# Kernel optimization log

Measured on AMD Instinct MI355X. Metric: run time of the kernel, lower is better.

The kernel has to match this reference:

```python
import jax, jax.numpy as jnp
import numpy as np

T, B, V, H = 2048, 32, 512, 512


def setup_inputs() -> dict:
    key = jax.random.key(0)
    ks = jax.random.split(key, 7)
    s = 1.0 / np.sqrt(V + H)  # torch nn.Linear default init bound
    u = lambda k, shape: jax.random.uniform(k, shape, jnp.float32, -s, s)
    return {
        "inputs": jax.random.normal(ks[0], (T, B, V), jnp.float32),
        "state": jnp.zeros((1, B, H), jnp.float32),
        "W_reset": u(ks[1], (V + H, H)),
        "b_reset": u(ks[2], (H,)),
        "W_net": u(ks[3], (V + H, H)),
        "b_net": u(ks[4], (H,)),
        "W_update": u(ks[5], (V + H, H)),
        "b_update": u(ks[6], (H,)),
    }


def reference(inputs, state, W_reset, b_reset, W_net, b_net, W_update, b_update):
    # inputs: [T, B, V], state: [1, B, H]
    h0 = state[0]  # [B, H]

    def step(h, x):
        # x: [B, V], h: [B, H]
        xh = jnp.concatenate([x, h], axis=-1)               # [B, V+H]
        R = jax.nn.sigmoid(xh @ W_reset + b_reset)          # [B, H]
        xr = jnp.concatenate([x, h * R], axis=-1)           # [B, V+H]
        H_t = jnp.tanh(xr @ W_net + b_net)                  # candidate
        Z = jax.nn.sigmoid(xr @ W_update + b_update)        # NOTE: from (x, h*R), faithful to source
        h_new = Z * h + (1.0 - Z) * H_t
        return h_new, h_new

    h_final, states = jax.lax.scan(step, h0, inputs)        # states: [T, B, H]
    return states, h_final[None]                            # ([T,B,H], [1,B,H])
```

## Files before the change

kernel.cpp:

```cpp
#include <hip/hip_runtime.h>
#include <cstdint>
#include <cstddef>

#define T_STEPS 2048
#define BATCH   32
#define VDIM    512
#define HDIM    512
#define SLICES  8
#define COLS    64
#define KPT     64
#define BM      128
#define BN      64

typedef _Float16 half2v __attribute__((ext_vector_type(2)));
typedef _Float16 half8v __attribute__((ext_vector_type(8)));
typedef float    f32x4  __attribute__((ext_vector_type(4)));

__device__ __forceinline__ float dot2h(half2v a, half2v b, float c) {
#if __has_builtin(__builtin_amdgcn_fdot2)
    return __builtin_amdgcn_fdot2(a, b, c, false);
#else
    return fmaf((float)a.x, (float)b.x, fmaf((float)a.y, (float)b.y, c));
#endif
}

__device__ __forceinline__ unsigned long long loadt(const unsigned long long* p) {
    return __hip_atomic_load(p, __ATOMIC_RELAXED, __HIP_MEMORY_SCOPE_AGENT);
}
__device__ __forceinline__ void storet(unsigned long long* p, float v, unsigned tag) {
    unsigned long long x = ((unsigned long long)tag << 32) | (unsigned)__float_as_uint(v);
    __hip_atomic_store(p, x, __ATOMIC_RELAXED, __HIP_MEMORY_SCOPE_AGENT);
}

__global__ __launch_bounds__(256)
void xproj_mfma(const float* __restrict__ X,
                const float* __restrict__ W0, const float* __restrict__ b0,
                const float* __restrict__ W1, const float* __restrict__ b1,
                const float* __restrict__ W2, const float* __restrict__ b2,
                float* __restrict__ xp, int M)
{
    const int g  = blockIdx.x >> 3;
    const int n0 = (blockIdx.x & 7) * BN;
    const int m0 = blockIdx.y * BM;
    const float* W    = (g == 0) ? W0 : (g == 1) ? W1 : W2;
    const float* bias = (g == 0) ? b0 : (g == 1) ? b1 : b2;
    float* out = xp + (size_t)g * M * HDIM;

    __shared__ __align__(16) _Float16 Blds[64 * 64 * 8];

    const int tid  = threadIdx.x;
    const int lane = tid & 63;
    const int w    = tid >> 6;
    const int r16  = lane & 15;
    const int kq   = lane >> 4;

    {
        const int c = tid & 63;
        #pragma unroll
        for (int it = 0; it < 16; ++it) {
            const int kg = (tid >> 6) + 4 * it;
            const float* src = W + (size_t)(kg * 8) * HDIM + n0 + c;
            half8v v;
            #pragma unroll
            for (int i = 0; i < 8; ++i) v[i] = (_Float16)src[(size_t)i * HDIM];
            *(half8v*)&Blds[(size_t)(kg * 64 + c) * 8] = v;
        }
    }
    __syncthreads();

    f32x4 acc[2][4] = {};

    for (int ks = 0; ks < 16; ++ks) {
        const int kg = 4 * ks + kq;
        half8v a[2];
        #pragma unroll
        for (int ms = 0; ms < 2; ++ms) {
            const float* ap = X + (size_t)(m0 + 32 * w + 16 * ms + r16) * VDIM + kg * 8;
            float4 a0 = *(const float4*)ap;
            float4 a1 = *(const float4*)(ap + 4);
            a[ms][0] = (_Float16)a0.x; a[ms][1] = (_Float16)a0.y;
            a[ms][2] = (_Float16)a0.z; a[ms][3] = (_Float16)a0.w;
            a[ms][4] = (_Float16)a1.x; a[ms][5] = (_Float16)a1.y;
            a[ms][6] = (_Float16)a1.z; a[ms][7] = (_Float16)a1.w;
        }
        #pragma unroll
        for (int cb = 0; cb < 4; ++cb) {
            half8v bf = *(const half8v*)&Blds[(size_t)(kg * 64 + 16 * cb + r16) * 8];
            acc[0][cb] = __builtin_amdgcn_mfma_f32_16x16x32_f16(a[0], bf, acc[0][cb], 0, 0, 0);
            acc[1][cb] = __builtin_amdgcn_mfma_f32_16x16x32_f16(a[1], bf, acc[1][cb], 0, 0, 0);
        }
    }

    #pragma unroll
    for (int cb = 0; cb < 4; ++cb) {
        const float bb = bias[n0 + 16 * cb + r16];
        #pragma unroll
        for (int ms = 0; ms < 2; ++ms)
            #pragma unroll
            for (int r = 0; r < 4; ++r) {
                const int row = m0 + 32 * w + 16 * ms + 4 * kq + r;
                out[(size_t)row * HDIM + n0 + 16 * cb + r16] = acc[ms][cb][r] + bb;
            }
    }
}

__global__ __launch_bounds__(512)
__attribute__((amdgpu_waves_per_eu(2, 2)))
void gru_scan3(const float* __restrict__ xp,
               const float* __restrict__ Wrh, const float* __restrict__ Wnh,
               const float* __restrict__ Wzh,
               const float* __restrict__ state, float* __restrict__ out,
               unsigned long long* __restrict__ hT,
               unsigned long long* __restrict__ uT,
               int t0, int nt, int M)
{
    const int b   = blockIdx.x & (BATCH - 1);
    const int s   = blockIdx.x >> 5;
    const int tid = threadIdx.x;
    const int c   = tid & (COLS - 1);
    const int j   = tid >> 6;
    const int n   = s * COLS + c;

    __shared__ __align__(16) _Float16 hlds[HDIM];
    __shared__ __align__(16) _Float16 ulds[HDIM];
    __shared__ float redR[SLICES][COLS];
    __shared__ float redN[SLICES][COLS];
    __shared__ float redZ[SLICES][COLS];

    half2v w2r[KPT / 2], w2n[KPT / 2], w2z[KPT / 2];
    {
        const size_t coloff = (size_t)s * COLS + c;
        const float* pr = Wrh + (size_t)j * KPT * HDIM + coloff;
        const float* pn = Wnh + (size_t)j * KPT * HDIM + coloff;
        const float* pz = Wzh + (size_t)j * KPT * HDIM + coloff;
        #pragma unroll
        for (int q = 0; q < KPT / 2; ++q) {
            half2v r, nn, z;
            r.x  = (_Float16)pr[(size_t)(2 * q) * HDIM];
            r.y  = (_Float16)pr[(size_t)(2 * q + 1) * HDIM];
            nn.x = (_Float16)pn[(size_t)(2 * q) * HDIM];
            nn.y = (_Float16)pn[(size_t)(2 * q + 1) * HDIM];
            z.x  = (_Float16)pz[(size_t)(2 * q) * HDIM];
            z.y  = (_Float16)pz[(size_t)(2 * q + 1) * HDIM];
            w2r[q] = r; w2n[q] = nn; w2z[q] = z;
        }
        #pragma unroll
        for (int q = 0; q < KPT / 2; ++q)
            asm volatile("" : "+v"(w2r[q]), "+v"(w2n[q]), "+v"(w2z[q]));
    }

    const size_t bb32 = (size_t)b * HDIM;
    unsigned long long* hTb = hT + bb32;
    unsigned long long* uTb = uT + bb32;
    const size_t gs = (size_t)M * HDIM;

    for (int tt = 0; tt < nt; ++tt) {
        const int t = t0 + tt;

        float xr = 0.f, xnn = 0.f, xz = 0.f;
        const size_t rb = ((size_t)tt * BATCH + b) * HDIM;
        if (tid < COLS) {
            xr  = xp[rb + n];
            xnn = xp[gs + rb + n];
            xz  = xp[2 * gs + rb + n];
        }

        float hv, hcv = 0.f;
        if (t == 0) {
            hv = state[bb32 + tid];
            if (tid < COLS) hcv = state[bb32 + n];
        } else {
            unsigned long long v;
            do { v = loadt(hTb + tid); } while ((unsigned)(v >> 32) != (unsigned)t);
            hv = __uint_as_float((unsigned)v);
            if (tid < COLS) {
                do { v = loadt(hTb + n); } while ((unsigned)(v >> 32) != (unsigned)t);
                hcv = __uint_as_float((unsigned)v);
            }
        }

        hlds[tid] = (_Float16)hv;
        asm volatile("s_waitcnt lgkmcnt(0)" ::: "memory");
        __builtin_amdgcn_sched_barrier(0);

        {
            float aR = 0.f;
            const half8v* hp = (const half8v*)&hlds[j * KPT];
            #pragma unroll
            for (int q = 0; q < KPT / 8; ++q) {
                half8v h8 = hp[q];
                half2v p0 = {h8[0], h8[1]}, p1 = {h8[2], h8[3]};
                half2v p2 = {h8[4], h8[5]}, p3 = {h8[6], h8[7]};
                aR = dot2h(p0, w2r[4 * q + 0], aR);
                aR = dot2h(p1, w2r[4 * q + 1], aR);
                aR = dot2h(p2, w2r[4 * q + 2], aR);
                aR = dot2h(p3, w2r[4 * q + 3], aR);
            }
            redR[j][c] = aR;
        }
        __syncthreads();

        if (tid < COLS) {
            float sR = 0.f;
            #pragma unroll
            for (int jj = 0; jj < SLICES; ++jj) sR += redR[jj][c];
            float R = 1.f / (1.f + __expf(-(xr + sR)));
            storet(uTb + n, hcv * R, (unsigned)(t + 1));
        }

        {
            unsigned long long v;
            do { v = loadt(uTb + tid); } while ((unsigned)(v >> 32) != (unsigned)(t + 1));
            ulds[tid] = (_Float16)__uint_as_float((unsigned)v);
        }
        asm volatile("s_waitcnt lgkmcnt(0)" ::: "memory");
        __builtin_amdgcn_sched_barrier(0);

        {
            float aN = 0.f, aZ = 0.f;
            const half8v* up = (const half8v*)&ulds[j * KPT];
            #pragma unroll
            for (int q = 0; q < KPT / 8; ++q) {
                half8v u8 = up[q];
                half2v p0 = {u8[0], u8[1]}, p1 = {u8[2], u8[3]};
                half2v p2 = {u8[4], u8[5]}, p3 = {u8[6], u8[7]};
                aN = dot2h(p0, w2n[4 * q + 0], aN);
                aZ = dot2h(p0, w2z[4 * q + 0], aZ);
                aN = dot2h(p1, w2n[4 * q + 1], aN);
                aZ = dot2h(p1, w2z[4 * q + 1], aZ);
                aN = dot2h(p2, w2n[4 * q + 2], aN);
                aZ = dot2h(p2, w2z[4 * q + 2], aZ);
                aN = dot2h(p3, w2n[4 * q + 3], aN);
                aZ = dot2h(p3, w2z[4 * q + 3], aZ);
            }
            redN[j][c] = aN;
            redZ[j][c] = aZ;
        }
        __syncthreads();

        if (tid < COLS) {
            float sN = 0.f, sZ = 0.f;
            #pragma unroll
            for (int jj = 0; jj < SLICES; ++jj) { sN += redN[jj][c]; sZ += redZ[jj][c]; }
            float e  = __expf(2.f * (xnn + sN));
            float Hc = 1.f - 2.f / (e + 1.f);
            float Z  = 1.f / (1.f + __expf(-(xz + sZ)));
            float hnew = Z * hcv + (1.f - Z) * Hc;
            __builtin_nontemporal_store(hnew, out + (size_t)t * BATCH * HDIM + bb32 + n);
            storet(hTb + n, hnew, (unsigned)(t + 1));
            if (t == T_STEPS - 1)
                out[(size_t)T_STEPS * BATCH * HDIM + bb32 + n] = hnew;
        }
    }
}

extern "C" void kernel_launch(void* const* d_in, const int* in_sizes, int n_in,
                              void* d_out, int out_size, void* d_ws, size_t ws_size,
                              hipStream_t stream) {
    const float* inputs   = (const float*)d_in[0];
    const float* state    = (const float*)d_in[1];
    const float* W_reset  = (const float*)d_in[2];
    const float* b_reset  = (const float*)d_in[3];
    const float* W_net    = (const float*)d_in[4];
    const float* b_net    = (const float*)d_in[5];
    const float* W_update = (const float*)d_in[6];
    const float* b_update = (const float*)d_in[7];
    float* out = (float*)d_out;

    const size_t tail_bytes = 2ull * BATCH * HDIM * 8;
    size_t tail_base = (ws_size - tail_bytes) & ~(size_t)255;
    char* base = (char*)d_ws;
    float* xp = (float*)base;
    unsigned long long* hT = (unsigned long long*)(base + tail_base);
    unsigned long long* uT = hT + (size_t)BATCH * HDIM;

    const size_t per_t = 3ull * BATCH * HDIM * sizeof(float);
    int C = (int)(tail_base / per_t);
    if (C > T_STEPS) C = T_STEPS;
    C &= ~3;
    if (C < 4) C = 4;

    hipMemsetAsync(hT, 0xFF, tail_bytes, stream);

    for (int t0 = 0; t0 < T_STEPS; t0 += C) {
        const int nt = (T_STEPS - t0 < C) ? (T_STEPS - t0) : C;
        const int M  = nt * BATCH;

        dim3 g1(8 * 3, M / BM);
        xproj_mfma<<<g1, 256, 0, stream>>>(inputs + (size_t)t0 * BATCH * VDIM,
                                           W_reset, b_reset,
                                           W_net,   b_net,
                                           W_update, b_update,
                                           xp, M);

        gru_scan3<<<BATCH * SLICES, 512, 0, stream>>>(
            xp,
            W_reset  + (size_t)VDIM * HDIM,
            W_net    + (size_t)VDIM * HDIM,
            W_update + (size_t)VDIM * HDIM,
            state, out, hT, uT, t0, nt, M);
    }
}
```

Baseline: 5.461 ms.

## Prepack fp16 weights, reuse X tile across gates, shorten scan critical path

A new pack kernel converts the input-projection weights to a packed fp16 layout once. The projection kernel then loads each block's X tile into registers a single time and loops over all three gates, staging each gate's B tile in LDS instead of re-reading and converting strided fp32 weights per block. In the recurrent scan, each owned h value is carried in a register instead of being re-polled every step, the dot-product and cross-slice reductions are split into independent partial sums to shorten dependency chains, and the h tag store is issued before the output store. The costs are a larger register footprint in the projection kernel and one extra kernel launch.

```diff
diff --git a/kernel.cpp b/kernel.cpp
--- a/kernel.cpp
+++ b/kernel.cpp
@@ -32,19 +32,29 @@
     __hip_atomic_store(p, x, __ATOMIC_RELAXED, __HIP_MEMORY_SCOPE_AGENT);
 }
 
+__global__ __launch_bounds__(512)
+void pack_b(const float* __restrict__ W0, const float* __restrict__ W1,
+            const float* __restrict__ W2, _Float16* __restrict__ Bt)
+{
+    const int kg = blockIdx.x;
+    const int g  = blockIdx.y;
+    const float* W = (g == 0) ? W0 : (g == 1) ? W1 : W2;
+    const int n = threadIdx.x;
+    half8v v;
+    #pragma unroll
+    for (int i = 0; i < 8; ++i)
+        v[i] = (_Float16)W[(size_t)(kg * 8 + i) * HDIM + n];
+    *(half8v*)&Bt[((((size_t)g * 64 + kg) * 512) + n) * 8] = v;
+}
+
 __global__ __launch_bounds__(256)
-void xproj_mfma(const float* __restrict__ X,
-                const float* __restrict__ W0, const float* __restrict__ b0,
-                const float* __restrict__ W1, const float* __restrict__ b1,
-                const float* __restrict__ W2, const float* __restrict__ b2,
-                float* __restrict__ xp, int M)
+void xproj_mfma2(const float* __restrict__ X, const _Float16* __restrict__ Bt,
+                 const float* __restrict__ b0, const float* __restrict__ b1,
+                 const float* __restrict__ b2,
+                 float* __restrict__ xp, int M)
 {
-    const int g  = blockIdx.x >> 3;
-    const int n0 = (blockIdx.x & 7) * BN;
+    const int n0 = blockIdx.x * BN;
     const int m0 = blockIdx.y * BM;
-    const float* W    = (g == 0) ? W0 : (g == 1) ? W1 : W2;
-    const float* bias = (g == 0) ? b0 : (g == 1) ? b1 : b2;
-    float* out = xp + (size_t)g * M * HDIM;
 
     __shared__ __align__(16) _Float16 Blds[64 * 64 * 8];
 
@@ -54,59 +64,74 @@
     const int r16  = lane & 15;
     const int kq   = lane >> 4;
 
-    {
-        const int c = tid & 63;
-        #pragma unroll
-        for (int it = 0; it < 16; ++it) {
-            const int kg = (tid >> 6) + 4 * it;
-            const float* src = W + (size_t)(kg * 8) * HDIM + n0 + c;
+    half8v a[2][16];
+    #pragma unroll
+    for (int ms = 0; ms < 2; ++ms) {
+        const float* ap = X + (size_t)(m0 + 32 * w + 16 * ms + r16) * VDIM;
+        #pragma unroll
+        for (int ks = 0; ks < 16; ++ks) {
+            const float* p = ap + ks * 32 + kq * 8;
+            float4 x0 = *(const float4*)p;
+            float4 x1 = *(const float4*)(p + 4);
             half8v v;
-            #pragma unroll
-            for (int i = 0; i < 8; ++i) v[i] = (_Float16)src[(size_t)i * HDIM];
-            *(half8v*)&Blds[(size_t)(kg * 64 + c) * 8] = v;
-        }
-    }
-    __syncthreads();
-
-    f32x4 acc[2][4] = {};
-
-    for (int ks = 0; ks < 16; ++ks) {
-        const int kg = 4 * ks + kq;
-        half8v a[2];
-        #pragma unroll
-        for (int ms = 0; ms < 2; ++ms) {
-            const float* ap = X + (size_t)(m0 + 32 * w + 16 * ms + r16) * VDIM + kg * 8;
-            float4 a0 = *(const float4*)ap;
-            float4 a1 = *(const float4*)(ap + 4);
-            a[ms][0] = (_Float16)a0.x; a[ms][1] = (_Float16)a0.y;
-            a[ms][2] = (_Float16)a0.z; a[ms][3] = (_Float16)a0.w;
-            a[ms][4] = (_Float16)a1.x; a[ms][5] = (_Float16)a1.y;
-            a[ms][6] = (_Float16)a1.z; a[ms][7] = (_Float16)a1.w;
-        }
+            v[0] = (_Float16)x0.x; v[1] = (_Float16)x0.y;
+            v[2] = (_Float16)x0.z; v[3] = (_Float16)x0.w;
+            v[4] = (_Float16)x1.x; v[5] = (_Float16)x1.y;
+            v[6] = (_Float16)x1.z; v[7] = (_Float16)x1.w;
+            a[ms][ks] = v;
+        }
+    }
+    #pragma unroll
+    for (int ms = 0; ms < 2; ++ms)
+        #pragma unroll
+        for (int ks = 0; ks < 16; ++ks)
+            asm volatile("" : "+v"(a[ms][ks]));
+
+    for (int g = 0; g < 3; ++g) {
+        __syncthreads();
+        {
+            const _Float16* src = Bt + (((size_t)g * 64) * 512 + n0) * 8;
+            const int c = tid & 63;
+            #pragma unroll
+            for (int it = 0; it < 16; ++it) {
+                const int kg = (tid >> 6) + 4 * it;
+                *(half8v*)&Blds[(size_t)(kg * 64 + c) * 8] =
+                    *(const half8v*)&src[((size_t)kg * 512 + c) * 8];
+            }
+        }
+        __syncthreads();
+
+        f32x4 acc[2][4] = {};
+        #pragma unroll
+        for (int ks = 0; ks < 16; ++ks) {
+            #pragma unroll
+            for (int cb = 0; cb < 4; ++cb) {
+                half8v bf = *(const half8v*)
+                    &Blds[(size_t)((4 * ks + kq) * 64 + 16 * cb + r16) * 8];
+                acc[0][cb] = __builtin_amdgcn_mfma_f32_16x16x32_f16(a[0][ks], bf, acc[0][cb], 0, 0, 0);
+                acc[1][cb] = __builtin_amdgcn_mfma_f32_16x16x32_f16(a[1][ks], bf, acc[1][cb], 0, 0, 0);
+            }
+        }
+
+        const float* bias = (g == 0) ? b0 : (g == 1) ? b1 : b2;
+        float* out = xp + (size_t)g * M * HDIM;
         #pragma unroll
         for (int cb = 0; cb < 4; ++cb) {
-            half8v bf = *(const half8v*)&Blds[(size_t)(kg * 64 + 16 * cb + r16) * 8];
-            acc[0][cb] = __builtin_amdgcn_mfma_f32_16x16x32_f16(a[0], bf, acc[0][cb], 0, 0, 0);
-            acc[1][cb] = __builtin_amdgcn_mfma_f32_16x16x32_f16(a[1], bf, acc[1][cb], 0, 0, 0);
-        }
-    }
-
-    #pragma unroll
-    for (int cb = 0; cb < 4; ++cb) {
-        const float bb = bias[n0 + 16 * cb + r16];
-        #pragma unroll
-        for (int ms = 0; ms < 2; ++ms)
-            #pragma unroll
-            for (int r = 0; r < 4; ++r) {
-                const int row = m0 + 32 * w + 16 * ms + 4 * kq + r;
-                out[(size_t)row * HDIM + n0 + 16 * cb + r16] = acc[ms][cb][r] + bb;
-            }
+            const float bb = bias[n0 + 16 * cb + r16];
+            #pragma unroll
+            for (int ms = 0; ms < 2; ++ms)
+                #pragma unroll
+                for (int r = 0; r < 4; ++r) {
+                    const int row = m0 + 32 * w + 16 * ms + 4 * kq + r;
+                    out[(size_t)row * HDIM + n0 + 16 * cb + r16] = acc[ms][cb][r] + bb;
+                }
+        }
     }
 }
 
 __global__ __launch_bounds__(512)
 __attribute__((amdgpu_waves_per_eu(2, 2)))
-void gru_scan3(const float* __restrict__ xp,
+void gru_scan6(const float* __restrict__ xp,
                const float* __restrict__ Wrh, const float* __restrict__ Wnh,
                const float* __restrict__ Wzh,
                const float* __restrict__ state, float* __restrict__ out,
@@ -154,6 +179,8 @@
     unsigned long long* uTb = uT + bb32;
     const size_t gs = (size_t)M * HDIM;
 
+    float hcv = 0.f;
+
     for (int tt = 0; tt < nt; ++tt) {
         const int t = t0 + tt;
 
@@ -165,7 +192,7 @@
             xz  = xp[2 * gs + rb + n];
         }
 
-        float hv, hcv = 0.f;
+        float hv;
         if (t == 0) {
             hv = state[bb32 + tid];
             if (tid < COLS) hcv = state[bb32 + n];
@@ -173,7 +200,7 @@
             unsigned long long v;
             do { v = loadt(hTb + tid); } while ((unsigned)(v >> 32) != (unsigned)t);
             hv = __uint_as_float((unsigned)v);
-            if (tid < COLS) {
+            if (tt == 0 && tid < COLS) {
                 do { v = loadt(hTb + n); } while ((unsigned)(v >> 32) != (unsigned)t);
                 hcv = __uint_as_float((unsigned)v);
             }
@@ -184,26 +211,28 @@
         __builtin_amdgcn_sched_barrier(0);
 
         {
-            float aR = 0.f;
+            float a0 = 0.f, a1 = 0.f, a2 = 0.f, a3 = 0.f;
             const half8v* hp = (const half8v*)&hlds[j * KPT];
             #pragma unroll
             for (int q = 0; q < KPT / 8; ++q) {
                 half8v h8 = hp[q];
                 half2v p0 = {h8[0], h8[1]}, p1 = {h8[2], h8[3]};
                 half2v p2 = {h8[4], h8[5]}, p3 = {h8[6], h8[7]};
-                aR = dot2h(p0, w2r[4 * q + 0], aR);
-                aR = dot2h(p1, w2r[4 * q + 1], aR);
-                aR = dot2h(p2, w2r[4 * q + 2], aR);
-                aR = dot2h(p3, w2r[4 * q + 3], aR);
-            }
-            redR[j][c] = aR;
+                a0 = dot2h(p0, w2r[4 * q + 0], a0);
+                a1 = dot2h(p1, w2r[4 * q + 1], a1);
+                a2 = dot2h(p2, w2r[4 * q + 2], a2);
+                a3 = dot2h(p3, w2r[4 * q + 3], a3);
+            }
+            redR[j][c] = (a0 + a1) + (a2 + a3);
         }
         __syncthreads();
 
         if (tid < COLS) {
-            float sR = 0.f;
-            #pragma unroll
-            for (int jj = 0; jj < SLICES; ++jj) sR += redR[jj][c];
+            float s01 = redR[0][c] + redR[1][c];
+            float s23 = redR[2][c] + redR[3][c];
+            float s45 = redR[4][c] + redR[5][c];
+            float s67 = redR[6][c] + redR[7][c];
+            float sR  = (s01 + s23) + (s45 + s67);
             float R = 1.f / (1.f + __expf(-(xr + sR)));
             storet(uTb + n, hcv * R, (unsigned)(t + 1));
         }
@@ -217,37 +246,41 @@
         __builtin_amdgcn_sched_barrier(0);
 
         {
-            float aN = 0.f, aZ = 0.f;
+            float aN0 = 0.f, aN1 = 0.f, aZ0 = 0.f, aZ1 = 0.f;
             const half8v* up = (const half8v*)&ulds[j * KPT];
             #pragma unroll
             for (int q = 0; q < KPT / 8; ++q) {
                 half8v u8 = up[q];
                 half2v p0 = {u8[0], u8[1]}, p1 = {u8[2], u8[3]};
                 half2v p2 = {u8[4], u8[5]}, p3 = {u8[6], u8[7]};
-                aN = dot2h(p0, w2n[4 * q + 0], aN);
-                aZ = dot2h(p0, w2z[4 * q + 0], aZ);
-                aN = dot2h(p1, w2n[4 * q + 1], aN);
-                aZ = dot2h(p1, w2z[4 * q + 1], aZ);
-                aN = dot2h(p2, w2n[4 * q + 2], aN);
-                aZ = dot2h(p2, w2z[4 * q + 2], aZ);
-                aN = dot2h(p3, w2n[4 * q + 3], aN);
-                aZ = dot2h(p3, w2z[4 * q + 3], aZ);
-            }
-            redN[j][c] = aN;
-            redZ[j][c] = aZ;
+                aN0 = dot2h(p0, w2n[4 * q + 0], aN0);
+                aZ0 = dot2h(p0, w2z[4 * q + 0], aZ0);
+                aN1 = dot2h(p1, w2n[4 * q + 1], aN1);
+                aZ1 = dot2h(p1, w2z[4 * q + 1], aZ1);
+                aN0 = dot2h(p2, w2n[4 * q + 2], aN0);
+                aZ0 = dot2h(p2, w2z[4 * q + 2], aZ0);
+                aN1 = dot2h(p3, w2n[4 * q + 3], aN1);
+                aZ1 = dot2h(p3, w2z[4 * q + 3], aZ1);
+            }
+            redN[j][c] = aN0 + aN1;
+            redZ[j][c] = aZ0 + aZ1;
         }
         __syncthreads();
 
         if (tid < COLS) {
-            float sN = 0.f, sZ = 0.f;
-            #pragma unroll
-            for (int jj = 0; jj < SLICES; ++jj) { sN += redN[jj][c]; sZ += redZ[jj][c]; }
+            float n01 = redN[0][c] + redN[1][c], n23 = redN[2][c] + redN[3][c];
+            float n45 = redN[4][c] + redN[5][c], n67 = redN[6][c] + redN[7][c];
+            float z01 = redZ[0][c] + redZ[1][c], z23 = redZ[2][c] + redZ[3][c];
+            float z45 = redZ[4][c] + redZ[5][c], z67 = redZ[6][c] + redZ[7][c];
+            float sN = (n01 + n23) + (n45 + n67);
+            float sZ = (z01 + z23) + (z45 + z67);
             float e  = __expf(2.f * (xnn + sN));
             float Hc = 1.f - 2.f / (e + 1.f);
             float Z  = 1.f / (1.f + __expf(-(xz + sZ)));
             float hnew = Z * hcv + (1.f - Z) * Hc;
+            storet(hTb + n, hnew, (unsigned)(t + 1));
             __builtin_nontemporal_store(hnew, out + (size_t)t * BATCH * HDIM + bb32 + n);
-            storet(hTb + n, hnew, (unsigned)(t + 1));
+            hcv = hnew;
             if (t == T_STEPS - 1)
                 out[(size_t)T_STEPS * BATCH * HDIM + bb32 + n] = hnew;
         }
@@ -267,33 +300,36 @@
     const float* b_update = (const float*)d_in[7];
     float* out = (float*)d_out;
 
-    const size_t tail_bytes = 2ull * BATCH * HDIM * 8;
-    size_t tail_base = (ws_size - tail_bytes) & ~(size_t)255;
+    const size_t tag_bytes = 2ull * BATCH * HDIM * 8;
+    const size_t bt_bytes  = 3ull * 64 * 512 * 8 * sizeof(_Float16);
+    size_t tag_base = (ws_size - tag_bytes) & ~(size_t)255;
+    size_t bt_base  = (tag_base - bt_bytes) & ~(size_t)255;
     char* base = (char*)d_ws;
-    float* xp = (float*)base;
-    unsigned long long* hT = (unsigned long long*)(base + tail_base);
+    float*      xp = (float*)base;
+    _Float16*   Bt = (_Float16*)(base + bt_base);
+    unsigned long long* hT = (unsigned long long*)(base + tag_base);
     unsigned long long* uT = hT + (size_t)BATCH * HDIM;
 
     const size_t per_t = 3ull * BATCH * HDIM * sizeof(float);
-    int C = (int)(tail_base / per_t);
+    int C = (int)(bt_base / per_t);
     if (C > T_STEPS) C = T_STEPS;
     C &= ~3;
     if (C < 4) C = 4;
 
-    hipMemsetAsync(hT, 0xFF, tail_bytes, stream);
+    hipMemsetAsync(hT, 0xFF, tag_bytes, stream);
+
+    dim3 gp(64, 3);
+    pack_b<<<gp, 512, 0, stream>>>(W_reset, W_net, W_update, Bt);
 
     for (int t0 = 0; t0 < T_STEPS; t0 += C) {
         const int nt = (T_STEPS - t0 < C) ? (T_STEPS - t0) : C;
         const int M  = nt * BATCH;
 
-        dim3 g1(8 * 3, M / BM);
-        xproj_mfma<<<g1, 256, 0, stream>>>(inputs + (size_t)t0 * BATCH * VDIM,
-                                           W_reset, b_reset,
-                                           W_net,   b_net,
-                                           W_update, b_update,
-                                           xp, M);
-
-        gru_scan3<<<BATCH * SLICES, 512, 0, stream>>>(
+        dim3 g1(HDIM / BN, M / BM);
+        xproj_mfma2<<<g1, 256, 0, stream>>>(inputs + (size_t)t0 * BATCH * VDIM,
+                                            Bt, b_reset, b_net, b_update, xp, M);
+
+        gru_scan6<<<BATCH * SLICES, 512, 0, stream>>>(
             xp,
             W_reset  + (size_t)VDIM * HDIM,
             W_net    + (size_t)VDIM * HDIM,
```

New measurement: 5.338 ms (median of 2 runs). -2.3%, faster.
